# Optimization experiments

Hardware: AMD Instinct MI355X
Metric: run time of the kernel (lower is better)

Reference implementation:

```python
import jax, jax.numpy as jnp
import numpy as np

EPS = 1e-5

def setup_inputs() -> dict:
    key = jax.random.key(0)
    ks = jax.random.split(key, 8)
    N, C, ST, LT = 32, 2048, 16, 400
    ALPHA, K, BETA, CK = 4, 3, 4, 3
    Cb = C // BETA
    inp = {
        'st_feat': jax.random.normal(ks[0], (N, C, ST, 1, 1), dtype=jnp.float32),
        'lt_feat': jax.random.normal(ks[1], (N, C, LT, 1, 1), dtype=jnp.float32),
        # global branch G: Linear(ST->ST*alpha) -> BN1d -> ReLU -> Linear(->K) -> softmax
        'g_w1': jax.random.normal(ks[2], (ST * ALPHA, ST), dtype=jnp.float32) * 0.02,
        'g_bn_gamma': jnp.ones((ST * ALPHA,), jnp.float32),
        'g_bn_beta': jnp.zeros((ST * ALPHA,), jnp.float32),
        'g_bn_mean': jnp.zeros((ST * ALPHA,), jnp.float32),
        'g_bn_var': jnp.ones((ST * ALPHA,), jnp.float32),
        'g_w2': jax.random.normal(ks[3], (K, ST * ALPHA), dtype=jnp.float32) * 0.02,
        # local branch L: Conv1d(C->C/beta,k=3) -> BN1d -> ReLU -> Conv1d(C/beta->C,1) -> sigmoid
        'l_w1': jax.random.normal(ks[4], (Cb, C, CK), dtype=jnp.float32) * 0.02,
        'l_bn_gamma': jnp.ones((Cb,), jnp.float32),
        'l_bn_beta': jnp.zeros((Cb,), jnp.float32),
        'l_bn_mean': jnp.zeros((Cb,), jnp.float32),
        'l_bn_var': jnp.ones((Cb,), jnp.float32),
        'l_w2': jax.random.normal(ks[5], (C, Cb), dtype=jnp.float32) * 0.02,
    }
    return inp


def reference(st_feat, lt_feat, g_w1, g_bn_gamma, g_bn_beta, g_bn_mean, g_bn_var,
              g_w2, l_w1, l_bn_gamma, l_bn_beta, l_bn_mean, l_bn_var, l_w2):
    N, C, ST = st_feat.shape[:3]
    LT = lt_feat.shape[2]
    K = g_w2.shape[0]
    PAD = 1  # adaptive_convolution_padding; stride = 1
    # ---- global branch: per-(n,c) adaptive kernel (h=w=1 so avgpool is identity)
    st = st_feat.reshape(N * C, ST)                               # [NC, ST]
    h = st @ g_w1.T                                               # [NC, ST*alpha]
    h = (h - g_bn_mean) * jax.lax.rsqrt(g_bn_var + EPS) * g_bn_gamma + g_bn_beta
    h = jax.nn.relu(h)
    conv_kernel = jax.nn.softmax(h @ g_w2.T, axis=-1)             # [NC, K]
    # ---- local branch: channel-temporal sigmoid gate
    lt = lt_feat.reshape(N, C, LT)                                # [N, C, LT]
    x = jax.lax.conv_general_dilated(lt, l_w1, window_strides=(1,),
                                     padding=[(1, 1)],
                                     dimension_numbers=('NCH', 'OIH', 'NCH'))  # [N, C/beta, LT]
    x = (x - l_bn_mean[None, :, None]) * jax.lax.rsqrt(l_bn_var + EPS)[None, :, None] \
        * l_bn_gamma[None, :, None] + l_bn_beta[None, :, None]
    x = jax.nn.relu(x)
    gate = jax.nn.sigmoid(jnp.einsum('oc,nct->not', l_w2, x))     # [N, C, LT]
    new_lt = lt * gate
    # ---- temporal adaptive aggregation: per-(n,c) depthwise 1D conv, K taps
    kern = conv_kernel.reshape(N, C, K)
    xp = jnp.pad(new_lt, ((0, 0), (0, 0), (PAD, PAD)))            # [N, C, LT+2*PAD]
    out_len = LT + 2 * PAD - K + 1                                # == LT for K=3, PAD=1
    out = jnp.zeros((N, C, out_len), dtype=new_lt.dtype)
    for i in range(K):  # K is tiny (3)
        out = out + kern[:, :, i:i + 1] * xp[:, :, i:i + out_len]
    return out.reshape(N, C, out_len, 1, 1)
```

## Files before the change

### kernel.cpp

```cpp
#include <hip/hip_runtime.h>
#include <hip/hip_bf16.h>

#define N_   32
#define C_   2048
#define ST_  16
#define H_   64
#define K_   3
#define CB_  512
#define LT_  400
#define LTP_ 402

using bf16x8 = __attribute__((ext_vector_type(8))) __bf16;
using f32x4  = __attribute__((ext_vector_type(4))) float;
typedef unsigned short ushort_t;

__device__ __forceinline__ unsigned short f2bf(float f) {
    unsigned int u = __float_as_uint(f);
    u = (u + 0x7fffu + ((u >> 16) & 1u)) >> 16;
    return (unsigned short)u;
}
__device__ __forceinline__ float bf2f(unsigned short h) {
    return __uint_as_float(((unsigned int)h) << 16);
}

__global__ __launch_bounds__(256) void k_global(
    const float* __restrict__ st, const float* __restrict__ g_w1,
    const float* __restrict__ gam, const float* __restrict__ bet,
    const float* __restrict__ mean, const float* __restrict__ var,
    const float* __restrict__ g_w2, float* __restrict__ kern) {
    __shared__ float w1[H_][ST_];
    __shared__ float sc[H_], bi[H_];
    __shared__ float w2[K_][H_];
    int tid = threadIdx.x;
    for (int i = tid; i < H_ * ST_; i += 256) w1[i / ST_][i % ST_] = g_w1[i];
    if (tid < H_) {
        float s = gam[tid] * rsqrtf(var[tid] + 1e-5f);
        sc[tid] = s;
        bi[tid] = bet[tid] - mean[tid] * s;
    }
    for (int i = tid; i < K_ * H_; i += 256) w2[i / H_][i % H_] = g_w2[i];
    __syncthreads();
    int row = blockIdx.x * 256 + tid;
    const float* p = st + (size_t)row * ST_;
    float s[ST_];
#pragma unroll
    for (int i = 0; i < ST_; ++i) s[i] = p[i];
    float lg0 = 0.f, lg1 = 0.f, lg2 = 0.f;
    for (int j = 0; j < H_; ++j) {
        float h = 0.f;
#pragma unroll
        for (int i = 0; i < ST_; ++i) h = fmaf(w1[j][i], s[i], h);
        h = fmaxf(fmaf(h, sc[j], bi[j]), 0.f);
        lg0 = fmaf(w2[0][j], h, lg0);
        lg1 = fmaf(w2[1][j], h, lg1);
        lg2 = fmaf(w2[2][j], h, lg2);
    }
    float m = fmaxf(lg0, fmaxf(lg1, lg2));
    float e0 = __expf(lg0 - m), e1 = __expf(lg1 - m), e2 = __expf(lg2 - m);
    float inv = 1.f / (e0 + e1 + e2);
    float4 o = make_float4(e0 * inv, e1 * inv, e2 * inv, 0.f);
    *(float4*)(kern + (size_t)row * 4) = o;
}

__global__ __launch_bounds__(256) void k_transpose(
    const float* __restrict__ lt, ushort_t* __restrict__ ltT) {
    __shared__ float tile[32][33];
    int tt = blockIdx.x * 32;
    int cc = blockIdx.y * 32;
    int n  = blockIdx.z;
    const float* src = lt + ((size_t)n * C_ + cc) * LT_;
    int tx = threadIdx.x & 31, ty = threadIdx.x >> 5;
#pragma unroll
    for (int i = 0; i < 4; ++i) {
        int c = ty + i * 8;
        int t = tt + tx;
        tile[c][tx] = (t < LT_) ? src[(size_t)c * LT_ + t] : 0.f;
    }
    __syncthreads();
    ushort_t* dst = ltT + (size_t)n * LTP_ * C_;
#pragma unroll
    for (int i = 0; i < 4; ++i) {
        int tl = ty + i * 8;
        int t = tt + tl;
        if (t < LT_) dst[(size_t)(t + 1) * C_ + cc + tx] = f2bf(tile[tx][tl]);
    }
}

__global__ __launch_bounds__(256) void k_zero(ushort_t* __restrict__ ltT) {
    int i = blockIdx.x * 256 + threadIdx.x;
    int n = i >> 11, c = i & (C_ - 1);
    size_t base = (size_t)n * LTP_ * C_;
    ltT[base + c] = 0;
    ltT[base + (size_t)(LTP_ - 1) * C_ + c] = 0;
}

__global__ __launch_bounds__(256) void k_w1(
    const float* __restrict__ l_w1, ushort_t* __restrict__ w1b) {
    int i = blockIdx.x * 256 + threadIdx.x;
    float a = l_w1[(size_t)i * 3 + 0];
    float b = l_w1[(size_t)i * 3 + 1];
    float c = l_w1[(size_t)i * 3 + 2];
    w1b[0 * (size_t)CB_ * C_ + i] = f2bf(a);
    w1b[1 * (size_t)CB_ * C_ + i] = f2bf(b);
    w1b[2 * (size_t)CB_ * C_ + i] = f2bf(c);
}

__global__ __launch_bounds__(256) void k_w2(
    const float* __restrict__ l_w2, ushort_t* __restrict__ w2b) {
    int i = blockIdx.x * 256 + threadIdx.x;
    w2b[i] = f2bf(l_w2[i]);
}

#define BK  32
#define AST 40

__global__ __launch_bounds__(256, 2) void k_gemm1(
    const ushort_t* __restrict__ ltT, const ushort_t* __restrict__ w1b,
    const float* __restrict__ bn_g, const float* __restrict__ bn_b,
    const float* __restrict__ bn_m, const float* __restrict__ bn_v,
    ushort_t* __restrict__ Xws) {
    __shared__ __align__(16) ushort_t Asm[130 * AST];
    __shared__ __align__(16) ushort_t Bsm[384 * AST];
    const int tid = threadIdx.x;
    const int n   = blockIdx.z;
    const int tm  = blockIdx.x * 128;
    const int cb0 = blockIdx.y * 128;
    const int lane = tid & 63, lrow = lane & 15, quad = lane >> 4;
    const int wv = tid >> 6, wvM = wv & 1, wvN = wv >> 1;

    f32x4 acc[4][4];
#pragma unroll
    for (int i = 0; i < 4; ++i)
#pragma unroll
        for (int j = 0; j < 4; ++j) acc[i][j] = (f32x4){0.f, 0.f, 0.f, 0.f};

    const int r0 = tid >> 2, q = tid & 3;
    const ushort_t* aSrc0 = ltT + ((size_t)n * LTP_ + min(tm + r0, LTP_ - 1)) * C_ + q * 8;
    const ushort_t* aSrc1 = ltT + ((size_t)n * LTP_ + min(tm + r0 + 64, LTP_ - 1)) * C_ + q * 8;
    const ushort_t* aSrc2 = ltT + ((size_t)n * LTP_ + min(tm + r0 + 128, LTP_ - 1)) * C_ + q * 8;
    ushort_t* aDst0 = Asm + r0 * AST + q * 8;
    ushort_t* aDst1 = Asm + (r0 + 64) * AST + q * 8;
    ushort_t* aDst2 = Asm + (r0 + 128) * AST + q * 8;
    const ushort_t* bSrc = w1b + (size_t)(cb0 + r0) * C_ + q * 8;
    ushort_t* bDst = Bsm + r0 * AST + q * 8;
    constexpr int OFFB[6] = {0, 64, 512, 576, 1024, 1088};

    for (int c0 = 0; c0 < C_; c0 += BK) {
        __syncthreads();
        *(uint4*)aDst0 = *(const uint4*)aSrc0;
        *(uint4*)aDst1 = *(const uint4*)aSrc1;
        if (tid < 8) *(uint4*)aDst2 = *(const uint4*)aSrc2;
#pragma unroll
        for (int i = 0; i < 6; ++i)
            *(uint4*)(bDst + i * 64 * AST) = *(const uint4*)(bSrc + (size_t)OFFB[i] * C_);
        aSrc0 += BK; aSrc1 += BK; aSrc2 += BK; bSrc += BK;
        __syncthreads();

        bf16x8 bfr[3][4];
#pragma unroll
        for (int k = 0; k < 3; ++k)
#pragma unroll
            for (int nf = 0; nf < 4; ++nf)
                bfr[k][nf] = *(const bf16x8*)&Bsm[(k * 128 + wvN * 64 + nf * 16 + lrow) * AST + quad * 8];
#pragma unroll
        for (int mf = 0; mf < 4; ++mf) {
            bf16x8 af[3];
#pragma unroll
            for (int k = 0; k < 3; ++k)
                af[k] = *(const bf16x8*)&Asm[(wvM * 64 + mf * 16 + lrow + k) * AST + quad * 8];
#pragma unroll
            for (int nf = 0; nf < 4; ++nf)
#pragma unroll
                for (int k = 0; k < 3; ++k)
                    acc[mf][nf] = __builtin_amdgcn_mfma_f32_16x16x32_bf16(af[k], bfr[k][nf], acc[mf][nf], 0, 0, 0);
        }
    }
    float s[4], bo[4];
#pragma unroll
    for (int nf = 0; nf < 4; ++nf) {
        int cb = cb0 + wvN * 64 + nf * 16 + lrow;
        float sc = bn_g[cb] * rsqrtf(bn_v[cb] + 1e-5f);
        s[nf] = sc;
        bo[nf] = bn_b[cb] - bn_m[cb] * sc;
    }
    const int tBase = tm + wvM * 64 + quad * 4;
#pragma unroll
    for (int mf = 0; mf < 4; ++mf) {
#pragma unroll
        for (int r = 0; r < 4; ++r) {
            int t = tBase + mf * 16 + r;
            if (t < LT_) {
#pragma unroll
                for (int nf = 0; nf < 4; ++nf) {
                    int cb = cb0 + wvN * 64 + nf * 16 + lrow;
                    float v = fmaxf(fmaf(acc[mf][nf][r], s[nf], bo[nf]), 0.f);
                    Xws[((size_t)n * LT_ + t) * CB_ + cb] = f2bf(v);
                }
            }
        }
    }
}

__global__ __launch_bounds__(256, 2) void k_gemm2(
    const ushort_t* __restrict__ Xws, const ushort_t* __restrict__ w2b,
    ushort_t* __restrict__ gate) {
    __shared__ __align__(16) ushort_t Asm[128 * AST];
    __shared__ __align__(16) ushort_t Bsm[128 * AST];
    const int tid = threadIdx.x;
    const int n  = blockIdx.z;
    const int cm = blockIdx.x * 128;
    const int tt = blockIdx.y * 128;
    const int lane = tid & 63, lrow = lane & 15, quad = lane >> 4;
    const int wv = tid >> 6, wvM = wv & 1, wvN = wv >> 1;

    f32x4 acc[4][4];
#pragma unroll
    for (int i = 0; i < 4; ++i)
#pragma unroll
        for (int j = 0; j < 4; ++j) acc[i][j] = (f32x4){0.f, 0.f, 0.f, 0.f};

    const int r0 = tid >> 2, q = tid & 3;
    const ushort_t* aSrc0 = w2b + (size_t)(cm + r0) * CB_ + q * 8;
    const ushort_t* aSrc1 = w2b + (size_t)(cm + r0 + 64) * CB_ + q * 8;
    const ushort_t* bSrc0 = Xws + ((size_t)n * LT_ + min(tt + r0, LT_ - 1)) * CB_ + q * 8;
    const ushort_t* bSrc1 = Xws + ((size_t)n * LT_ + min(tt + r0 + 64, LT_ - 1)) * CB_ + q * 8;
    ushort_t* aDst0 = Asm + r0 * AST + q * 8;
    ushort_t* aDst1 = Asm + (r0 + 64) * AST + q * 8;
    ushort_t* bDst0 = Bsm + r0 * AST + q * 8;
    ushort_t* bDst1 = Bsm + (r0 + 64) * AST + q * 8;

    for (int k0 = 0; k0 < CB_; k0 += BK) {
        __syncthreads();
        *(uint4*)aDst0 = *(const uint4*)aSrc0;
        *(uint4*)aDst1 = *(const uint4*)aSrc1;
        *(uint4*)bDst0 = *(const uint4*)bSrc0;
        *(uint4*)bDst1 = *(const uint4*)bSrc1;
        aSrc0 += BK; aSrc1 += BK; bSrc0 += BK; bSrc1 += BK;
        __syncthreads();

        bf16x8 af[4], bfm[4];
#pragma unroll
        for (int mf = 0; mf < 4; ++mf)
            af[mf] = *(const bf16x8*)&Asm[(wvM * 64 + mf * 16 + lrow) * AST + quad * 8];
#pragma unroll
        for (int nf = 0; nf < 4; ++nf)
            bfm[nf] = *(const bf16x8*)&Bsm[(wvN * 64 + nf * 16 + lrow) * AST + quad * 8];
#pragma unroll
        for (int mf = 0; mf < 4; ++mf)
#pragma unroll
            for (int nf = 0; nf < 4; ++nf)
                acc[mf][nf] = __builtin_amdgcn_mfma_f32_16x16x32_bf16(af[mf], bfm[nf], acc[mf][nf], 0, 0, 0);
    }
#pragma unroll
    for (int mf = 0; mf < 4; ++mf) {
#pragma unroll
        for (int r = 0; r < 4; ++r) {
            int c = cm + wvM * 64 + mf * 16 + quad * 4 + r;
#pragma unroll
            for (int nf = 0; nf < 4; ++nf) {
                int t = tt + wvN * 64 + nf * 16 + lrow;
                if (t < LT_) {
                    float g = 1.f / (1.f + __expf(-acc[mf][nf][r]));
                    gate[((size_t)n * C_ + c) * LT_ + t] = f2bf(g);
                }
            }
        }
    }
}

__global__ __launch_bounds__(256) void k_final(
    const float* __restrict__ lt, const ushort_t* __restrict__ gate,
    const float* __restrict__ kern, float* __restrict__ out) {
    long long idx = (long long)blockIdx.x * 256 + threadIdx.x;
    int t0 = (int)(idx % 100) * 4;
    long long nc = idx / 100;
    const float*   ltp = lt   + (size_t)nc * LT_;
    const ushort_t* gp = gate + (size_t)nc * LT_;
    float4 kv = *(const float4*)(kern + (size_t)nc * 4);
    float nl[6];
#pragma unroll
    for (int j = -1; j <= 4; ++j) {
        int t = t0 + j;
        nl[j + 1] = (t >= 0 && t < LT_) ? ltp[t] * bf2f(gp[t]) : 0.f;
    }
    float4 o;
    o.x = kv.x * nl[0] + kv.y * nl[1] + kv.z * nl[2];
    o.y = kv.x * nl[1] + kv.y * nl[2] + kv.z * nl[3];
    o.z = kv.x * nl[2] + kv.y * nl[3] + kv.z * nl[4];
    o.w = kv.x * nl[3] + kv.y * nl[4] + kv.z * nl[5];
    *(float4*)(out + (size_t)nc * LT_ + t0) = o;
}

extern "C" void kernel_launch(void* const* d_in, const int* in_sizes, int n_in,
                              void* d_out, int out_size, void* d_ws, size_t ws_size,
                              hipStream_t stream) {
    const float* st   = (const float*)d_in[0];
    const float* lt   = (const float*)d_in[1];
    const float* g_w1 = (const float*)d_in[2];
    const float* g_bg = (const float*)d_in[3];
    const float* g_bb = (const float*)d_in[4];
    const float* g_bm = (const float*)d_in[5];
    const float* g_bv = (const float*)d_in[6];
    const float* g_w2 = (const float*)d_in[7];
    const float* l_w1 = (const float*)d_in[8];
    const float* l_bg = (const float*)d_in[9];
    const float* l_bb = (const float*)d_in[10];
    const float* l_bm = (const float*)d_in[11];
    const float* l_bv = (const float*)d_in[12];
    const float* l_w2 = (const float*)d_in[13];
    float* out = (float*)d_out;

    char* ws = (char*)d_ws;
    float*    kern = (float*)(ws + 0);
    ushort_t* w1b  = (ushort_t*)(ws + 1048576);
    ushort_t* w2b  = (ushort_t*)(ws + 7340032);
    ushort_t* Xws  = (ushort_t*)(ws + 9437184);
    ushort_t* ltT  = (ushort_t*)(ws + 22544384);
    ushort_t* gate = ltT;

    k_global<<<dim3((N_ * C_) / 256), dim3(256), 0, stream>>>(
        st, g_w1, g_bg, g_bb, g_bm, g_bv, g_w2, kern);
    k_w1<<<dim3((CB_ * C_) / 256), dim3(256), 0, stream>>>(l_w1, w1b);
    k_w2<<<dim3((C_ * CB_) / 256), dim3(256), 0, stream>>>(l_w2, w2b);
    k_zero<<<dim3((N_ * C_) / 256), dim3(256), 0, stream>>>(ltT);
    k_transpose<<<dim3(13, C_ / 32, N_), dim3(256), 0, stream>>>(lt, ltT);
    k_gemm1<<<dim3(4, 4, N_), dim3(256), 0, stream>>>(
        ltT, w1b, l_bg, l_bb, l_bm, l_bv, Xws);
    k_gemm2<<<dim3(C_ / 128, 4, N_), dim3(256), 0, stream>>>(Xws, w2b, gate);
    k_final<<<dim3((N_ * C_ * (LT_ / 4)) / 256), dim3(256), 0, stream>>>(
        lt, gate, kern, out);
}
```

Measured before the change: 446.3 us.

## Double-buffer GEMM tiles via direct global-to-LDS loads with XOR swizzle

```diff
diff --git a/kernel.cpp b/kernel.cpp
--- a/kernel.cpp
+++ b/kernel.cpp
@@ -9,6 +9,8 @@
 #define CB_  512
 #define LT_  400
 #define LTP_ 402
+#define BK   32
+#define TSTR 126
 
 using bf16x8 = __attribute__((ext_vector_type(8))) __bf16;
 using f32x4  = __attribute__((ext_vector_type(4))) float;
@@ -21,6 +23,11 @@
 }
 __device__ __forceinline__ float bf2f(unsigned short h) {
     return __uint_as_float(((unsigned int)h) << 16);
+}
+__device__ __forceinline__ void gload16(const ushort_t* g, ushort_t* l) {
+    __builtin_amdgcn_global_load_lds(
+        (const __attribute__((address_space(1))) unsigned int*)g,
+        (__attribute__((address_space(3))) unsigned int*)l, 16, 0, 0);
 }
 
 __global__ __launch_bounds__(256) void k_global(
@@ -65,24 +72,30 @@
 __global__ __launch_bounds__(256) void k_transpose(
     const float* __restrict__ lt, ushort_t* __restrict__ ltT) {
     __shared__ float tile[32][33];
-    int tt = blockIdx.x * 32;
-    int cc = blockIdx.y * 32;
-    int n  = blockIdx.z;
+    int tt0 = blockIdx.x * 32;
+    int cc  = blockIdx.y * 32;
+    int n   = blockIdx.z;
     const float* src = lt + ((size_t)n * C_ + cc) * LT_;
     int tx = threadIdx.x & 31, ty = threadIdx.x >> 5;
 #pragma unroll
     for (int i = 0; i < 4; ++i) {
         int c = ty + i * 8;
-        int t = tt + tx;
+        int t = tt0 + tx;
         tile[c][tx] = (t < LT_) ? src[(size_t)c * LT_ + t] : 0.f;
     }
     __syncthreads();
-    ushort_t* dst = ltT + (size_t)n * LTP_ * C_;
-#pragma unroll
-    for (int i = 0; i < 4; ++i) {
-        int tl = ty + i * 8;
-        int t = tt + tl;
-        if (t < LT_) dst[(size_t)(t + 1) * C_ + cc + tx] = f2bf(tile[tx][tl]);
+    int cx  = (threadIdx.x & 15) * 2;
+    int tyw = threadIdx.x >> 4;
+    unsigned int* dst = (unsigned int*)(ltT + (size_t)n * LTP_ * C_ + cc + cx);
+#pragma unroll
+    for (int i = 0; i < 2; ++i) {
+        int tl = tyw + i * 16;
+        int t = tt0 + tl;
+        if (t < LT_) {
+            unsigned int v = (unsigned int)f2bf(tile[cx][tl]) |
+                             ((unsigned int)f2bf(tile[cx + 1][tl]) << 16);
+            dst[(size_t)(t + 1) * (C_ / 2)] = v;
+        }
     }
 }
 
@@ -111,63 +124,80 @@
     w2b[i] = f2bf(l_w2[i]);
 }
 
-#define BK  32
-#define AST 40
-
 __global__ __launch_bounds__(256, 2) void k_gemm1(
     const ushort_t* __restrict__ ltT, const ushort_t* __restrict__ w1b,
     const float* __restrict__ bn_g, const float* __restrict__ bn_b,
     const float* __restrict__ bn_m, const float* __restrict__ bn_v,
     ushort_t* __restrict__ Xws) {
-    __shared__ __align__(16) ushort_t Asm[130 * AST];
-    __shared__ __align__(16) ushort_t Bsm[384 * AST];
+    __shared__ __align__(16) ushort_t Asm[2 * 128 * BK];
+    __shared__ __align__(16) ushort_t Bsm[2 * 384 * BK];
     const int tid = threadIdx.x;
     const int n   = blockIdx.z;
-    const int tm  = blockIdx.x * 128;
+    const int tm  = blockIdx.x * TSTR;
     const int cb0 = blockIdx.y * 128;
     const int lane = tid & 63, lrow = lane & 15, quad = lane >> 4;
     const int wv = tid >> 6, wvM = wv & 1, wvN = wv >> 1;
 
+    const int srow = lane >> 2;
+    const int csrc = (((lane & 3) ^ ((lane >> 3) & 3)) << 3);
+    const ushort_t* gA[2];
+#pragma unroll
+    for (int i = 0; i < 2; ++i) {
+        int r = (2 * wv + i) * 16 + srow;
+        int gr = tm + r; gr = gr < LTP_ - 1 ? gr : LTP_ - 1;
+        gA[i] = ltT + ((size_t)n * LTP_ + gr) * C_ + csrc;
+    }
+    const ushort_t* gB[6];
+#pragma unroll
+    for (int j = 0; j < 6; ++j) {
+        int r = (6 * wv + j) * 16 + srow;
+        gB[j] = w1b + ((size_t)((r >> 7) * CB_ + cb0 + (r & 127))) * C_ + csrc;
+    }
+    const int sB = lrow * BK + ((quad ^ ((lrow >> 1) & 3)) << 3);
+    int sA[3];
+#pragma unroll
+    for (int k = 0; k < 3; ++k)
+        sA[k] = (lrow + k) * BK + ((quad ^ (((lrow + k) >> 1) & 3)) << 3);
+
     f32x4 acc[4][4];
 #pragma unroll
     for (int i = 0; i < 4; ++i)
 #pragma unroll
         for (int j = 0; j < 4; ++j) acc[i][j] = (f32x4){0.f, 0.f, 0.f, 0.f};
 
-    const int r0 = tid >> 2, q = tid & 3;
-    const ushort_t* aSrc0 = ltT + ((size_t)n * LTP_ + min(tm + r0, LTP_ - 1)) * C_ + q * 8;
-    const ushort_t* aSrc1 = ltT + ((size_t)n * LTP_ + min(tm + r0 + 64, LTP_ - 1)) * C_ + q * 8;
-    const ushort_t* aSrc2 = ltT + ((size_t)n * LTP_ + min(tm + r0 + 128, LTP_ - 1)) * C_ + q * 8;
-    ushort_t* aDst0 = Asm + r0 * AST + q * 8;
-    ushort_t* aDst1 = Asm + (r0 + 64) * AST + q * 8;
-    ushort_t* aDst2 = Asm + (r0 + 128) * AST + q * 8;
-    const ushort_t* bSrc = w1b + (size_t)(cb0 + r0) * C_ + q * 8;
-    ushort_t* bDst = Bsm + r0 * AST + q * 8;
-    constexpr int OFFB[6] = {0, 64, 512, 576, 1024, 1088};
-
-    for (int c0 = 0; c0 < C_; c0 += BK) {
+#define STAGE1(buf)                                                         \
+    {                                                                       \
+        ushort_t* ad = Asm + (buf) * (128 * BK) + (2 * wv) * (16 * BK);     \
+        gload16(gA[0], ad);                                                 \
+        gload16(gA[1], ad + 16 * BK);                                       \
+        gA[0] += BK; gA[1] += BK;                                           \
+        ushort_t* bd = Bsm + (buf) * (384 * BK) + (6 * wv) * (16 * BK);     \
+        _Pragma("unroll")                                                   \
+        for (int j = 0; j < 6; ++j) {                                       \
+            gload16(gB[j], bd + j * (16 * BK));                             \
+            gB[j] += BK;                                                    \
+        }                                                                   \
+    }
+
+    STAGE1(0);
+    for (int s = 0; s < C_ / BK; ++s) {
         __syncthreads();
-        *(uint4*)aDst0 = *(const uint4*)aSrc0;
-        *(uint4*)aDst1 = *(const uint4*)aSrc1;
-        if (tid < 8) *(uint4*)aDst2 = *(const uint4*)aSrc2;
-#pragma unroll
-        for (int i = 0; i < 6; ++i)
-            *(uint4*)(bDst + i * 64 * AST) = *(const uint4*)(bSrc + (size_t)OFFB[i] * C_);
-        aSrc0 += BK; aSrc1 += BK; aSrc2 += BK; bSrc += BK;
-        __syncthreads();
-
+        const int cur = s & 1;
+        if (s + 1 < C_ / BK) STAGE1(cur ^ 1);
+        const ushort_t* Ab = Asm + cur * (128 * BK) + wvM * (64 * BK);
+        const ushort_t* Bb = Bsm + cur * (384 * BK) + wvN * (64 * BK) + sB;
         bf16x8 bfr[3][4];
 #pragma unroll
         for (int k = 0; k < 3; ++k)
 #pragma unroll
             for (int nf = 0; nf < 4; ++nf)
-                bfr[k][nf] = *(const bf16x8*)&Bsm[(k * 128 + wvN * 64 + nf * 16 + lrow) * AST + quad * 8];
+                bfr[k][nf] = *(const bf16x8*)(Bb + k * (128 * BK) + nf * (16 * BK));
 #pragma unroll
         for (int mf = 0; mf < 4; ++mf) {
             bf16x8 af[3];
 #pragma unroll
             for (int k = 0; k < 3; ++k)
-                af[k] = *(const bf16x8*)&Asm[(wvM * 64 + mf * 16 + lrow + k) * AST + quad * 8];
+                af[k] = *(const bf16x8*)(Ab + sA[k] + mf * (16 * BK));
 #pragma unroll
             for (int nf = 0; nf < 4; ++nf)
 #pragma unroll
@@ -175,25 +205,26 @@
                     acc[mf][nf] = __builtin_amdgcn_mfma_f32_16x16x32_bf16(af[k], bfr[k][nf], acc[mf][nf], 0, 0, 0);
         }
     }
-    float s[4], bo[4];
+#undef STAGE1
+    float sc[4], bo[4];
 #pragma unroll
     for (int nf = 0; nf < 4; ++nf) {
         int cb = cb0 + wvN * 64 + nf * 16 + lrow;
-        float sc = bn_g[cb] * rsqrtf(bn_v[cb] + 1e-5f);
-        s[nf] = sc;
-        bo[nf] = bn_b[cb] - bn_m[cb] * sc;
-    }
-    const int tBase = tm + wvM * 64 + quad * 4;
+        float s0 = bn_g[cb] * rsqrtf(bn_v[cb] + 1e-5f);
+        sc[nf] = s0;
+        bo[nf] = bn_b[cb] - bn_m[cb] * s0;
+    }
 #pragma unroll
     for (int mf = 0; mf < 4; ++mf) {
 #pragma unroll
         for (int r = 0; r < 4; ++r) {
-            int t = tBase + mf * 16 + r;
-            if (t < LT_) {
+            int local = wvM * 64 + mf * 16 + quad * 4 + r;
+            int t = tm + local;
+            if (local < TSTR && t < LT_) {
 #pragma unroll
                 for (int nf = 0; nf < 4; ++nf) {
                     int cb = cb0 + wvN * 64 + nf * 16 + lrow;
-                    float v = fmaxf(fmaf(acc[mf][nf][r], s[nf], bo[nf]), 0.f);
+                    float v = fmaxf(fmaf(acc[mf][nf][r], sc[nf], bo[nf]), 0.f);
                     Xws[((size_t)n * LT_ + t) * CB_ + cb] = f2bf(v);
                 }
             }
@@ -201,11 +232,11 @@
     }
 }
 
-__global__ __launch_bounds__(256, 2) void k_gemm2(
+__global__ __launch_bounds__(256, 3) void k_gemm2(
     const ushort_t* __restrict__ Xws, const ushort_t* __restrict__ w2b,
     ushort_t* __restrict__ gate) {
-    __shared__ __align__(16) ushort_t Asm[128 * AST];
-    __shared__ __align__(16) ushort_t Bsm[128 * AST];
+    __shared__ __align__(16) ushort_t Asm[2 * 128 * BK];
+    __shared__ __align__(16) ushort_t Bsm[2 * 128 * BK];
     const int tid = threadIdx.x;
     const int n  = blockIdx.z;
     const int cm = blockIdx.x * 128;
@@ -213,44 +244,57 @@
     const int lane = tid & 63, lrow = lane & 15, quad = lane >> 4;
     const int wv = tid >> 6, wvM = wv & 1, wvN = wv >> 1;
 
+    const int srow = lane >> 2;
+    const int csrc = (((lane & 3) ^ ((lane >> 3) & 3)) << 3);
+    const ushort_t* gA[2];
+    const ushort_t* gB[2];
+#pragma unroll
+    for (int i = 0; i < 2; ++i) {
+        int r = (2 * wv + i) * 16 + srow;
+        gA[i] = w2b + (size_t)(cm + r) * CB_ + csrc;
+        int tr = tt + r; tr = tr < LT_ - 1 ? tr : LT_ - 1;
+        gB[i] = Xws + ((size_t)n * LT_ + tr) * CB_ + csrc;
+    }
+    const int sOff = lrow * BK + ((quad ^ ((lrow >> 1) & 3)) << 3);
+
     f32x4 acc[4][4];
 #pragma unroll
     for (int i = 0; i < 4; ++i)
 #pragma unroll
         for (int j = 0; j < 4; ++j) acc[i][j] = (f32x4){0.f, 0.f, 0.f, 0.f};
 
-    const int r0 = tid >> 2, q = tid & 3;
-    const ushort_t* aSrc0 = w2b + (size_t)(cm + r0) * CB_ + q * 8;
-    const ushort_t* aSrc1 = w2b + (size_t)(cm + r0 + 64) * CB_ + q * 8;
-    const ushort_t* bSrc0 = Xws + ((size_t)n * LT_ + min(tt + r0, LT_ - 1)) * CB_ + q * 8;
-    const ushort_t* bSrc1 = Xws + ((size_t)n * LT_ + min(tt + r0 + 64, LT_ - 1)) * CB_ + q * 8;
-    ushort_t* aDst0 = Asm + r0 * AST + q * 8;
-    ushort_t* aDst1 = Asm + (r0 + 64) * AST + q * 8;
-    ushort_t* bDst0 = Bsm + r0 * AST + q * 8;
-    ushort_t* bDst1 = Bsm + (r0 + 64) * AST + q * 8;
-
-    for (int k0 = 0; k0 < CB_; k0 += BK) {
+#define STAGE2(buf)                                                         \
+    {                                                                       \
+        ushort_t* ad = Asm + (buf) * (128 * BK) + (2 * wv) * (16 * BK);     \
+        ushort_t* bd = Bsm + (buf) * (128 * BK) + (2 * wv) * (16 * BK);     \
+        gload16(gA[0], ad);                                                 \
+        gload16(gA[1], ad + 16 * BK);                                       \
+        gload16(gB[0], bd);                                                 \
+        gload16(gB[1], bd + 16 * BK);                                       \
+        gA[0] += BK; gA[1] += BK; gB[0] += BK; gB[1] += BK;                 \
+    }
+
+    STAGE2(0);
+    for (int s = 0; s < CB_ / BK; ++s) {
         __syncthreads();
-        *(uint4*)aDst0 = *(const uint4*)aSrc0;
-        *(uint4*)aDst1 = *(const uint4*)aSrc1;
-        *(uint4*)bDst0 = *(const uint4*)bSrc0;
-        *(uint4*)bDst1 = *(const uint4*)bSrc1;
-        aSrc0 += BK; aSrc1 += BK; bSrc0 += BK; bSrc1 += BK;
-        __syncthreads();
-
+        const int cur = s & 1;
+        if (s + 1 < CB_ / BK) STAGE2(cur ^ 1);
+        const ushort_t* Ab = Asm + cur * (128 * BK) + wvM * (64 * BK) + sOff;
+        const ushort_t* Bb = Bsm + cur * (128 * BK) + wvN * (64 * BK) + sOff;
         bf16x8 af[4], bfm[4];
 #pragma unroll
         for (int mf = 0; mf < 4; ++mf)
-            af[mf] = *(const bf16x8*)&Asm[(wvM * 64 + mf * 16 + lrow) * AST + quad * 8];
+            af[mf] = *(const bf16x8*)(Ab + mf * (16 * BK));
 #pragma unroll
         for (int nf = 0; nf < 4; ++nf)
-            bfm[nf] = *(const bf16x8*)&Bsm[(wvN * 64 + nf * 16 + lrow) * AST + quad * 8];
+            bfm[nf] = *(const bf16x8*)(Bb + nf * (16 * BK));
 #pragma unroll
         for (int mf = 0; mf < 4; ++mf)
 #pragma unroll
             for (int nf = 0; nf < 4; ++nf)
                 acc[mf][nf] = __builtin_amdgcn_mfma_f32_16x16x32_bf16(af[mf], bfm[nf], acc[mf][nf], 0, 0, 0);
     }
+#undef STAGE2
 #pragma unroll
     for (int mf = 0; mf < 4; ++mf) {
 #pragma unroll
```

Measured after the change: 425.1 us. -4.7%, faster.
